# Kernel optimization log

Hardware: AMD Instinct MI355X
Metric: run time of the kernel (lower is better)

Reference implementation:

```python
import jax, jax.numpy as jnp
import numpy as np

N = 50000
DIN, DH, DOUT = 128, 128, 64
DEPTH = 3
TEMP = 1.0
WEIGHT = 0.5
LN_EPS = 1e-5
E_RAND = 1_600_000


def setup_inputs() -> dict:
    key = jax.random.key(0)
    ks = jax.random.split(key, 16)
    x = jax.random.normal(ks[0], (N, DIN), jnp.float32)
    # random edges + ring (guarantees degree >= 2 after symmetrization)
    src = jax.random.randint(ks[1], (E_RAND,), 0, N)
    dst = jax.random.randint(ks[2], (E_RAND,), 0, N)
    ring = jnp.arange(N)
    s = jnp.concatenate([src, ring])
    d = jnp.concatenate([dst, (ring + 1) % N])
    edge_index = jnp.stack([jnp.concatenate([s, d]), jnp.concatenate([d, s])]).astype(jnp.int64)  # [2, 3.3M], symmetric

    def glorot(k, i, o):
        return jax.random.normal(k, (i, o), jnp.float32) * jnp.sqrt(2.0 / (i + o)).astype(jnp.float32)

    return {
        "x": x, "edge_index": edge_index,
        "W0": glorot(ks[3], DIN, DH), "b0": jnp.zeros((DH,), jnp.float32),
        "W1": glorot(ks[4], DH, DH),  "b1": jnp.zeros((DH,), jnp.float32),
        "W2": glorot(ks[5], DH, DH),  "b2": jnp.zeros((DH,), jnp.float32),
        "W_out": glorot(ks[6], DH, DOUT), "b_out": jnp.zeros((DOUT,), jnp.float32),
        "gamma": jnp.ones((DH,), jnp.float32), "beta": jnp.zeros((DH,), jnp.float32),
    }


def _seg(vals, idx):
    return jax.ops.segment_sum(vals, idx, num_segments=N)


def _gcn_conv(h_in, W, b, src, dst):
    # PyG GCNConv: self-loops, sym norm D^-1/2 (A+I) D^-1/2
    h = h_in @ W
    ones = jnp.ones(src.shape, jnp.float32)
    deg = _seg(ones, dst) + 1.0  # degree incl. self-loop
    dinv = jax.lax.rsqrt(deg)
    msg = h[src] * (dinv[src] * dinv[dst])[:, None]
    return _seg(msg, dst) + h * (1.0 / deg)[:, None] + b


def _layernorm(x, g, b):
    m = jnp.mean(x, axis=-1, keepdims=True)
    v = jnp.mean((x - m) ** 2, axis=-1, keepdims=True)
    return (x - m) * jax.lax.rsqrt(v + LN_EPS) * g + b


def reference(x, edge_index, W0, b0, W1, b1, W2, b2, W_out, b_out, gamma, beta):
    src, dst = edge_index[0], edge_index[1]
    h = x
    for W, b in ((W0, b0), (W1, b1), (W2, b2)):
        h = _layernorm(jax.nn.relu(_gcn_conv(h, W, b, src, dst)), gamma, beta)
    emb = _gcn_conv(h, W_out, b_out, src, dst)  # [N, DOUT]

    # --- entropy gradient (edge-list form of the dense-A einsums) ---
    ones = jnp.ones(src.shape, jnp.float32)
    deg_adj = _seg(ones, src)                     # row sums of A (no self-loops)
    en_norm = 1.0 / jnp.sqrt(deg_adj * DH)        # uses hidden_dim, as in the original

    rn2 = jnp.sum(emb * emb, axis=1)              # ||X_i||^2
    dot = jnp.sum(emb[src] * emb[dst], axis=1)    # <X_i, X_j> per edge
    res1 = deg_adj * rn2
    res2 = _seg(dot, src)
    res3 = _seg(rn2[dst], src)
    energies = 0.5 * (res1 - 2.0 * res2 + res3) * en_norm  # normalize_energies=True

    logits = -energies / TEMP
    P = jax.nn.softmax(logits, axis=0) + 1e-10
    logP = jnp.log(P)
    S = -jnp.sum(P * logP)
    Pbar = P * (S + logP)                         # [N]

    nsumX = _seg(emb[dst], src)                   # sum_j A_ij X_j
    nsumP = _seg(Pbar[dst], src)                  # sum_j A_ij Pbar_j
    XP = emb * Pbar[:, None]
    g1 = deg_adj[:, None] * XP
    g2 = emb * nsumP[:, None]
    g3 = Pbar[:, None] * nsumX
    g4 = _seg(XP[dst], src)
    grad_S = (g1 + g2 - g3 - g4) / TEMP * en_norm[:, None]

    return emb + WEIGHT * grad_S
```

## Files before the change

### kernel.cpp

```cpp
#include <hip/hip_runtime.h>

#define DIN 128
#define DH  128
#define DFO 64
#define LN_EPS 1e-5f
#define WEIGHT 0.5f

#define MAXB  104
#define CAPB  64
#define FLUSH 32
#define SENT  0xFFFFFFFFu

typedef unsigned int uint32;

__device__ __forceinline__ float bf_lo(uint32 u) { return __uint_as_float(u << 16); }
__device__ __forceinline__ float bf_hi(uint32 u) { return __uint_as_float(u & 0xFFFF0000u); }
__device__ __forceinline__ uint32 pack_bf16(float a, float b) {
  uint32 ua = __float_as_uint(a), ub = __float_as_uint(b);
  ua += 0x7FFFu + ((ua >> 16) & 1u);
  ub += 0x7FFFu + ((ub >> 16) & 1u);
  return (ua >> 16) | (ub & 0xFFFF0000u);
}

__device__ __forceinline__ float wave_sum(float v) {
  #pragma unroll
  for (int off = 32; off > 0; off >>= 1) v += __shfl_xor(v, off);
  return v;
}
__device__ __forceinline__ float wave_max(float v) {
  #pragma unroll
  for (int off = 32; off > 0; off >>= 1) v = fmaxf(v, __shfl_xor(v, off));
  return v;
}

__device__ __forceinline__ void acc8(float* a, uint4 u) {
  a[0] += bf_lo(u.x); a[1] += bf_hi(u.x);
  a[2] += bf_lo(u.y); a[3] += bf_hi(u.y);
  a[4] += bf_lo(u.z); a[5] += bf_hi(u.z);
  a[6] += bf_lo(u.w); a[7] += bf_hi(u.w);
}
__device__ __forceinline__ void fma8(float* a, uint4 u, float p) {
  a[0] = fmaf(bf_lo(u.x), p, a[0]); a[1] = fmaf(bf_hi(u.x), p, a[1]);
  a[2] = fmaf(bf_lo(u.y), p, a[2]); a[3] = fmaf(bf_hi(u.y), p, a[3]);
  a[4] = fmaf(bf_lo(u.z), p, a[4]); a[5] = fmaf(bf_hi(u.z), p, a[5]);
  a[6] = fmaf(bf_lo(u.w), p, a[6]); a[7] = fmaf(bf_hi(u.w), p, a[7]);
}

__global__ __launch_bounds__(256) void k_bin3(const int* __restrict__ src, const int* __restrict__ dst,
                       int E2, int nbc, int GCAP, int* __restrict__ gbcnt,
                       uint32* __restrict__ gpairs) {
  __shared__ uint32 lbuf[MAXB][CAPB];
  __shared__ int lcnt[MAXB];
  __shared__ int fbase[MAXB];
  __shared__ int fm[MAXB];
  __shared__ short flist[MAXB];
  __shared__ int fn;
  int wv = threadIdx.x >> 6, ln = threadIdx.x & 63;
  for (int b = threadIdx.x; b < nbc; b += 256) lcnt[b] = 0;
  __syncthreads();

  for (int base = blockIdx.x * 256; base < E2; base += gridDim.x * 256) {
    int i = base + threadIdx.x;
    if (i < E2) {
      int s = src[i], d = dst[i];
      int b0 = s >> 9;
      uint32 v0 = ((uint32)(s & 511) << 16) | (uint32)d;
      int sl = atomicAdd(&lcnt[b0], 1);
      if (sl < CAPB) lbuf[b0][sl] = v0;
      else { int g = atomicAdd(&gbcnt[b0 * 16], 1); gpairs[(size_t)b0 * GCAP + g] = v0; }
      int b1 = d >> 9;
      uint32 v1 = ((uint32)(d & 511) << 16) | (uint32)s;
      sl = atomicAdd(&lcnt[b1], 1);
      if (sl < CAPB) lbuf[b1][sl] = v1;
      else { int g = atomicAdd(&gbcnt[b1 * 16], 1); gpairs[(size_t)b1 * GCAP + g] = v1; }
    }
    if (threadIdx.x == 0) fn = 0;
    __syncthreads();
    if (threadIdx.x < nbc) {
      int m = lcnt[threadIdx.x];
      if (m >= FLUSH) {
        if (m > CAPB) m = CAPB;
        int r = (m + 15) & ~15;
        fbase[threadIdx.x] = atomicAdd(&gbcnt[threadIdx.x * 16], r);
        fm[threadIdx.x] = m;
        int fi = atomicAdd(&fn, 1);
        flist[fi] = (short)threadIdx.x;
      }
    }
    __syncthreads();
    int nf = fn;
    for (int fi = wv; fi < nf; fi += 4) {
      int b = flist[fi];
      int m = fm[b], r = (m + 15) & ~15, g = fbase[b];
      if (ln < r)
        gpairs[(size_t)b * GCAP + g + ln] = (ln < m) ? lbuf[b][ln] : SENT;
    }
    __syncthreads();
    if (threadIdx.x < nbc && lcnt[threadIdx.x] >= FLUSH) lcnt[threadIdx.x] = 0;
    __syncthreads();
  }
  if (threadIdx.x < nbc) {
    int m = lcnt[threadIdx.x]; if (m > CAPB) m = CAPB;
    fm[threadIdx.x] = m;
    if (m > 0) {
      int r = (m + 15) & ~15;
      fbase[threadIdx.x] = atomicAdd(&gbcnt[threadIdx.x * 16], r);
    }
  }
  __syncthreads();
  for (int b = wv; b < nbc; b += 4) {
    int m = fm[b];
    if (m > 0) {
      int r = (m + 15) & ~15, g = fbase[b];
      if (ln < r)
        gpairs[(size_t)b * GCAP + g + ln] = (ln < m) ? lbuf[b][ln] : SENT;
    }
  }
}

__global__ __launch_bounds__(1024) void k_csr(const uint32* __restrict__ gpairs, const int* __restrict__ gbcnt,
                      int GCAP, int GCAPC, int N, int* __restrict__ rowbeg, int* __restrict__ rowcnt,
                      float* __restrict__ dinv, float* __restrict__ cntf, int* __restrict__ col) {
  __shared__ int hist[512];
  __shared__ int pos[512];
  int b = blockIdx.x, tid = threadIdx.x;
  if (tid < 512) hist[tid] = 0;
  __syncthreads();
  int m = gbcnt[b * 16];
  const uint32* pp = gpairs + (size_t)b * GCAP;
  for (int t = tid; t < m; t += 1024) {
    uint32 v = pp[t];
    if (v != SENT) atomicAdd(&hist[v >> 16], 1);
  }
  __syncthreads();
  int cnt = (tid < 512) ? hist[tid] : 0;
  for (int off = 1; off < 512; off <<= 1) {
    int u = (tid >= off && tid < 512) ? hist[tid - off] : 0;
    __syncthreads();
    if (tid < 512) hist[tid] += u;
    __syncthreads();
  }
  int cbase = b * GCAPC;
  if (tid < 512) {
    int excl = hist[tid] - cnt;
    pos[tid] = excl;
    int node = (b << 9) + tid;
    if (node < N) {
      rowbeg[node] = cbase + excl;
      rowcnt[node] = cnt;
      cntf[node] = (float)cnt;
      dinv[node] = rsqrtf((float)cnt + 1.0f);
    }
  }
  __syncthreads();
  for (int t = tid; t < m; t += 1024) {
    uint32 v = pp[t];
    if (v != SENT) {
      int sl = atomicAdd(&pos[v >> 16], 1);
      col[cbase + sl] = (int)(v & 0xFFFFu);
    }
  }
}

template <int COLS, bool BF16A>
__global__ __launch_bounds__(256) void k_gemm_tile(const void* __restrict__ Ap, const float* __restrict__ W,
                            const float* __restrict__ dinv, uint32* __restrict__ outb, int N) {
  const int CG  = COLS / 4;
  const int RG  = 256 / CG;
  const int RPT = 64 / RG;
  __shared__ float4 At4[64 * 32];
  int t = threadIdx.x;
  int rbase = blockIdx.x * 64;
  #pragma unroll
  for (int i2 = 0; i2 < 8; ++i2) {
    int idx = t + 256 * i2;
    int row = idx >> 5, c4i = idx & 31;
    int gr = rbase + row;
    float4 v = make_float4(0.f, 0.f, 0.f, 0.f);
    if (gr < N) {
      if (BF16A) {
        uint2 p = ((const uint2*)Ap)[(size_t)gr * 32 + c4i];
        v = make_float4(bf_lo(p.x), bf_hi(p.x), bf_lo(p.y), bf_hi(p.y));
      } else {
        v = ((const float4*)Ap)[(size_t)gr * 32 + c4i];
      }
    }
    At4[idx] = v;
  }
  __syncthreads();
  int c4 = t % CG, rg = t / CG;
  float acc[RPT][4];
  #pragma unroll
  for (int r = 0; r < RPT; ++r) { acc[r][0] = acc[r][1] = acc[r][2] = acc[r][3] = 0.f; }
  const float4* W4 = (const float4*)W;
  #pragma unroll 2
  for (int k4 = 0; k4 < 32; ++k4) {
    float4 w0 = W4[(k4 * 4 + 0) * CG + c4];
    float4 w1 = W4[(k4 * 4 + 1) * CG + c4];
    float4 w2 = W4[(k4 * 4 + 2) * CG + c4];
    float4 w3 = W4[(k4 * 4 + 3) * CG + c4];
    #pragma unroll
    for (int r = 0; r < RPT; ++r) {
      float4 av = At4[(rg * RPT + r) * 32 + k4];
      acc[r][0] = fmaf(av.x, w0.x, acc[r][0]); acc[r][0] = fmaf(av.y, w1.x, acc[r][0]);
      acc[r][0] = fmaf(av.z, w2.x, acc[r][0]); acc[r][0] = fmaf(av.w, w3.x, acc[r][0]);
      acc[r][1] = fmaf(av.x, w0.y, acc[r][1]); acc[r][1] = fmaf(av.y, w1.y, acc[r][1]);
      acc[r][1] = fmaf(av.z, w2.y, acc[r][1]); acc[r][1] = fmaf(av.w, w3.y, acc[r][1]);
      acc[r][2] = fmaf(av.x, w0.z, acc[r][2]); acc[r][2] = fmaf(av.y, w1.z, acc[r][2]);
      acc[r][2] = fmaf(av.z, w2.z, acc[r][2]); acc[r][2] = fmaf(av.w, w3.z, acc[r][2]);
      acc[r][3] = fmaf(av.x, w0.w, acc[r][3]); acc[r][3] = fmaf(av.y, w1.w, acc[r][3]);
      acc[r][3] = fmaf(av.z, w2.w, acc[r][3]); acc[r][3] = fmaf(av.w, w3.w, acc[r][3]);
    }
  }
  #pragma unroll
  for (int r = 0; r < RPT; ++r) {
    int gr = rbase + rg * RPT + r;
    if (gr < N) {
      float s = dinv[gr];
      uint2 o;
      o.x = pack_bf16(acc[r][0] * s, acc[r][1] * s);
      o.y = pack_bf16(acc[r][2] * s, acc[r][3] * s);
      ((uint2*)outb)[(size_t)gr * CG + c4] = o;
    }
  }
}

__global__ __launch_bounds__(128) void k_agg_ln(const uint4* __restrict__ hsb4, const int* __restrict__ rowbeg,
                         const int* __restrict__ rowcnt, const int* __restrict__ col,
                         const float* __restrict__ dinv, const float* __restrict__ bias,
                         const float* __restrict__ gamma, const float* __restrict__ beta,
                         uint4* __restrict__ hout, int N) {
  int i = blockIdx.x;
  int tid = threadIdx.x;
  int lane = tid & 63;
  int f4 = lane & 15;
  int sl = ((tid >> 6) << 2) | (lane >> 4);
  int beg = rowbeg[i], end = beg + rowcnt[i];
  float a[8] = {0,0,0,0,0,0,0,0}, b[8] = {0,0,0,0,0,0,0,0};
  if (tid < 16) { uint4 u = hsb4[(size_t)i * 16 + f4]; acc8(a, u); }
  int t = beg + sl;
  for (; t + 8 < end; t += 16) {
    int j0 = col[t], j1 = col[t + 8];
    uint4 u0 = hsb4[(size_t)j0 * 16 + f4];
    uint4 u1 = hsb4[(size_t)j1 * 16 + f4];
    acc8(a, u0); acc8(b, u1);
  }
  for (; t < end; t += 8) {
    int j = col[t];
    uint4 u = hsb4[(size_t)j * 16 + f4];
    acc8(a, u);
  }
  #pragma unroll
  for (int k = 0; k < 8; ++k) {
    a[k] += b[k];
    a[k] += __shfl_xor(a[k], 16);
    a[k] += __shfl_xor(a[k], 32);
  }
  __shared__ float4 part[16][2];
  if (tid >= 64 && tid < 80) {
    part[f4][0] = make_float4(a[0], a[1], a[2], a[3]);
    part[f4][1] = make_float4(a[4], a[5], a[6], a[7]);
  }
  __syncthreads();
  if (tid < 16) {
    float4 p0 = part[f4][0], p1 = part[f4][1];
    a[0] += p0.x; a[1] += p0.y; a[2] += p0.z; a[3] += p0.w;
    a[4] += p1.x; a[5] += p1.y; a[6] += p1.z; a[7] += p1.w;
    float di = dinv[i];
    float4 bb0 = ((const float4*)bias)[f4 * 2], bb1 = ((const float4*)bias)[f4 * 2 + 1];
    float v[8];
    v[0] = fmaxf(fmaf(a[0], di, bb0.x), 0.f);
    v[1] = fmaxf(fmaf(a[1], di, bb0.y), 0.f);
    v[2] = fmaxf(fmaf(a[2], di, bb0.z), 0.f);
    v[3] = fmaxf(fmaf(a[3], di, bb0.w), 0.f);
    v[4] = fmaxf(fmaf(a[4], di, bb1.x), 0.f);
    v[5] = fmaxf(fmaf(a[5], di, bb1.y), 0.f);
    v[6] = fmaxf(fmaf(a[6], di, bb1.z), 0.f);
    v[7] = fmaxf(fmaf(a[7], di, bb1.w), 0.f);
    float s = 0.f, s2 = 0.f;
    #pragma unroll
    for (int k = 0; k < 8; ++k) { s += v[k]; s2 += v[k] * v[k]; }
    #pragma unroll
    for (int off = 8; off > 0; off >>= 1) { s += __shfl_xor(s, off); s2 += __shfl_xor(s2, off); }
    float mean = s * (1.f / 128.f);
    float var  = s2 * (1.f / 128.f) - mean * mean;
    float rstd = rsqrtf(var + LN_EPS);
    float4 gg0 = ((const float4*)gamma)[f4 * 2], gg1 = ((const float4*)gamma)[f4 * 2 + 1];
    float4 be0 = ((const float4*)beta)[f4 * 2],  be1 = ((const float4*)beta)[f4 * 2 + 1];
    float g0 = (v[0] - mean) * rstd * gg0.x + be0.x;
    float g1 = (v[1] - mean) * rstd * gg0.y + be0.y;
    float g2 = (v[2] - mean) * rstd * gg0.z + be0.z;
    float g3 = (v[3] - mean) * rstd * gg0.w + be0.w;
    float g4 = (v[4] - mean) * rstd * gg1.x + be1.x;
    float g5 = (v[5] - mean) * rstd * gg1.y + be1.y;
    float g6 = (v[6] - mean) * rstd * gg1.z + be1.z;
    float g7 = (v[7] - mean) * rstd * gg1.w + be1.w;
    uint4 o;
    o.x = pack_bf16(g0, g1); o.y = pack_bf16(g2, g3);
    o.z = pack_bf16(g4, g5); o.w = pack_bf16(g6, g7);
    hout[(size_t)i * 16 + f4] = o;
  }
}

__global__ __launch_bounds__(64) void k_agg_out(const uint4* __restrict__ hso4, const int* __restrict__ rowbeg,
                          const int* __restrict__ rowcnt, const int* __restrict__ col,
                          const float* __restrict__ dinv, const float* __restrict__ bias,
                          float* __restrict__ embf, uint4* __restrict__ embb4,
                          float* __restrict__ rn2, int N) {
  int i = blockIdx.x, lane = threadIdx.x;
  int f4 = lane & 7, sl = lane >> 3;
  int beg = rowbeg[i], end = beg + rowcnt[i];
  float a[8] = {0,0,0,0,0,0,0,0}, b[8] = {0,0,0,0,0,0,0,0};
  if (lane < 8) { uint4 u = hso4[(size_t)i * 8 + f4]; acc8(a, u); }
  int t = beg + sl;
  for (; t + 8 < end; t += 16) {
    int j0 = col[t], j1 = col[t + 8];
    uint4 u0 = hso4[(size_t)j0 * 8 + f4];
    uint4 u1 = hso4[(size_t)j1 * 8 + f4];
    acc8(a, u0); acc8(b, u1);
  }
  for (; t < end; t += 8) {
    uint4 u = hso4[(size_t)col[t] * 8 + f4];
    acc8(a, u);
  }
  #pragma unroll
  for (int k = 0; k < 8; ++k) {
    a[k] += b[k];
    a[k] += __shfl_xor(a[k], 8);
    a[k] += __shfl_xor(a[k], 16);
    a[k] += __shfl_xor(a[k], 32);
  }
  float di = dinv[i];
  float4 bb0 = ((const float4*)bias)[f4 * 2], bb1 = ((const float4*)bias)[f4 * 2 + 1];
  float e[8];
  e[0] = fmaf(a[0], di, bb0.x); e[1] = fmaf(a[1], di, bb0.y);
  e[2] = fmaf(a[2], di, bb0.z); e[3] = fmaf(a[3], di, bb0.w);
  e[4] = fmaf(a[4], di, bb1.x); e[5] = fmaf(a[5], di, bb1.y);
  e[6] = fmaf(a[6], di, bb1.z); e[7] = fmaf(a[7], di, bb1.w);
  float ss = 0.f;
  #pragma unroll
  for (int k = 0; k < 8; ++k) ss += e[k] * e[k];
  ss += __shfl_xor(ss, 1); ss += __shfl_xor(ss, 2); ss += __shfl_xor(ss, 4);
  if (lane == 0) rn2[i] = ss;
  if (lane < 8) {
    ((float4*)embf)[(size_t)i * 16 + f4 * 2]     = make_float4(e[0], e[1], e[2], e[3]);
    ((float4*)embf)[(size_t)i * 16 + f4 * 2 + 1] = make_float4(e[4], e[5], e[6], e[7]);
    uint4 o;
    o.x = pack_bf16(e[0], e[1]); o.y = pack_bf16(e[2], e[3]);
    o.z = pack_bf16(e[4], e[5]); o.w = pack_bf16(e[6], e[7]);
    embb4[(size_t)i * 8 + f4] = o;
  }
}

__global__ __launch_bounds__(64) void k_passA(const float* __restrict__ embf, const uint4* __restrict__ embb4,
                        const int* __restrict__ rowbeg, const int* __restrict__ rowcnt,
                        const int* __restrict__ col, const float* __restrict__ rn2,
                        const float* __restrict__ cntf, float* __restrict__ nsumX,
                        float* __restrict__ logits, int N) {
  int i = blockIdx.x, lane = threadIdx.x;
  int f4 = lane & 7, sl = lane >> 3;
  int beg = rowbeg[i], end = beg + rowcnt[i];
  float a[8] = {0,0,0,0,0,0,0,0}, b[8] = {0,0,0,0,0,0,0,0};
  float r3 = 0.f;
  int t = beg + sl;
  for (; t + 8 < end; t += 16) {
    int j0 = col[t], j1 = col[t + 8];
    uint4 u0 = embb4[(size_t)j0 * 8 + f4];
    uint4 u1 = embb4[(size_t)j1 * 8 + f4];
    acc8(a, u0); acc8(b, u1);
    if (f4 == 0) r3 += rn2[j0] + rn2[j1];
  }
  for (; t < end; t += 8) {
    int j = col[t];
    uint4 u = embb4[(size_t)j * 8 + f4];
    acc8(a, u);
    if (f4 == 0) r3 += rn2[j];
  }
  #pragma unroll
  for (int k = 0; k < 8; ++k) {
    a[k] += b[k];
    a[k] += __shfl_xor(a[k], 8);
    a[k] += __shfl_xor(a[k], 16);
    a[k] += __shfl_xor(a[k], 32);
  }
  r3 += __shfl_xor(r3, 8); r3 += __shfl_xor(r3, 16); r3 += __shfl_xor(r3, 32);
  float4 e0 = ((const float4*)embf)[(size_t)i * 16 + f4 * 2];
  float4 e1 = ((const float4*)embf)[(size_t)i * 16 + f4 * 2 + 1];
  float dd = e0.x * a[0] + e0.y * a[1] + e0.z * a[2] + e0.w * a[3]
           + e1.x * a[4] + e1.y * a[5] + e1.z * a[6] + e1.w * a[7];
  dd += __shfl_xor(dd, 1); dd += __shfl_xor(dd, 2); dd += __shfl_xor(dd, 4);
  r3 += __shfl_xor(r3, 1); r3 += __shfl_xor(r3, 2); r3 += __shfl_xor(r3, 4);
  if (lane < 8) {
    ((float4*)nsumX)[(size_t)i * 16 + f4 * 2]     = make_float4(a[0], a[1], a[2], a[3]);
    ((float4*)nsumX)[(size_t)i * 16 + f4 * 2 + 1] = make_float4(a[4], a[5], a[6], a[7]);
  }
  if (lane == 0) {
    float c = cntf[i];
    float en = rsqrtf(c * 128.0f);
    logits[i] = -0.5f * (c * rn2[i] - 2.f * dd + r3) * en;
  }
}

__global__ __launch_bounds__(256) void k_sm1(const float* __restrict__ logits, int N,
                                             float4* __restrict__ partials) {
  int idx = blockIdx.x * 256 + threadIdx.x;
  int w = threadIdx.x >> 6, ln = threadIdx.x & 63;
  float x = (idx < N) ? logits[idx] : -3.4e38f;
  float m = wave_max(x);
  __shared__ float red[3][4];
  if (ln == 0) red[0][w] = m;
  __syncthreads();
  float M = fmaxf(fmaxf(red[0][0], red[0][1]), fmaxf(red[0][2], red[0][3]));
  float ev = (idx < N) ? expf(x - M) : 0.f;
  float tv = (idx < N) ? (x - M) * ev : 0.f;
  float se = wave_sum(ev), st = wave_sum(tv);
  if (ln == 0) { red[1][w] = se; red[2][w] = st; }
  __syncthreads();
  if (threadIdx.x == 0)
    partials[blockIdx.x] = make_float4(M, red[1][0] + red[1][1] + red[1][2] + red[1][3],
                                          red[2][0] + red[2][1] + red[2][2] + red[2][3], 0.f);
}

__global__ __launch_bounds__(256) void k_sm2(const float4* __restrict__ partials, int nb,
                                             float* __restrict__ scal) {
  int tid = threadIdx.x;
  int w = tid >> 6, ln = tid & 63;
  float4 p = (tid < nb) ? partials[tid] : make_float4(-3.4e38f, 0.f, 0.f, 0.f);
  float m = wave_max(p.x);
  __shared__ float red[3][4];
  if (ln == 0) red[0][w] = m;
  __syncthreads();
  float M = fmaxf(fmaxf(red[0][0], red[0][1]), fmaxf(red[0][2], red[0][3]));
  float sc = (tid < nb) ? expf(p.x - M) : 0.f;
  float se = p.y * sc;
  float tt = (p.z + (p.x - M) * p.y) * sc;
  se = wave_sum(se); tt = wave_sum(tt);
  if (ln == 0) { red[1][w] = se; red[2][w] = tt; }
  __syncthreads();
  if (tid == 0) {
    float SE = red[1][0] + red[1][1] + red[1][2] + red[1][3];
    float TT = red[2][0] + red[2][1] + red[2][2] + red[2][3];
    scal[0] = M;
    scal[1] = SE;
    scal[2] = logf(SE) - TT / SE;
  }
}

__global__ __launch_bounds__(256) void k_pbar(const float* __restrict__ logits, int N,
                     const float* __restrict__ scal, float* __restrict__ Pb) {
  float M = scal[0], SE = scal[1], S = scal[2];
  int i = blockIdx.x * blockDim.x + threadIdx.x;
  int stride = gridDim.x * blockDim.x;
  for (; i < N; i += stride) {
    float p = expf(logits[i] - M) / SE + 1e-10f;
    Pb[i] = p * (S + logf(p));
  }
}

__global__ __launch_bounds__(64) void k_passB(const float* __restrict__ embf, const uint4* __restrict__ embb4,
                        const int* __restrict__ rowbeg, const int* __restrict__ rowcnt,
                        const int* __restrict__ col, const float* __restrict__ Pb,
                        const float* __restrict__ cntf, float* __restrict__ outp, int N) {
  int i = blockIdx.x, lane = threadIdx.x;
  int f4 = lane & 7, sl = lane >> 3;
  int beg = rowbeg[i], end = beg + rowcnt[i];
  float a[8] = {0,0,0,0,0,0,0,0}, b[8] = {0,0,0,0,0,0,0,0};
  float sp = 0.f;
  int t = beg + sl;
  for (; t + 8 < end; t += 16) {
    int j0 = col[t], j1 = col[t + 8];
    float p0 = Pb[j0], p1 = Pb[j1];
    uint4 u0 = embb4[(size_t)j0 * 8 + f4];
    uint4 u1 = embb4[(size_t)j1 * 8 + f4];
    fma8(a, u0, p0); fma8(b, u1, p1);
    if (f4 == 0) sp += p0 + p1;
  }
  for (; t < end; t += 8) {
    int j = col[t];
    float p = Pb[j];
    uint4 u = embb4[(size_t)j * 8 + f4];
    fma8(a, u, p);
    if (f4 == 0) sp += p;
  }
  #pragma unroll
  for (int k = 0; k < 8; ++k) {
    a[k] += b[k];
    a[k] += __shfl_xor(a[k], 8);
    a[k] += __shfl_xor(a[k], 16);
    a[k] += __shfl_xor(a[k], 32);
  }
  sp += __shfl_xor(sp, 8); sp += __shfl_xor(sp, 16); sp += __shfl_xor(sp, 32);
  sp += __shfl_xor(sp, 1); sp += __shfl_xor(sp, 2); sp += __shfl_xor(sp, 4);
  if (lane < 8) {
    float4 e0 = ((const float4*)embf)[(size_t)i * 16 + f4 * 2];
    float4 e1 = ((const float4*)embf)[(size_t)i * 16 + f4 * 2 + 1];
    float4 n0 = ((const float4*)outp)[(size_t)i * 16 + f4 * 2];
    float4 n1 = ((const float4*)outp)[(size_t)i * 16 + f4 * 2 + 1];
    float Pi = Pb[i];
    float c = cntf[i];
    float wgt = WEIGHT * rsqrtf(c * 128.0f);
    float g0 = c * e0.x * Pi + e0.x * sp - Pi * n0.x - a[0];
    float g1 = c * e0.y * Pi + e0.y * sp - Pi * n0.y - a[1];
    float g2 = c * e0.z * Pi + e0.z * sp - Pi * n0.z - a[2];
    float g3 = c * e0.w * Pi + e0.w * sp - Pi * n0.w - a[3];
    float g4 = c * e1.x * Pi + e1.x * sp - Pi * n1.x - a[4];
    float g5 = c * e1.y * Pi + e1.y * sp - Pi * n1.y - a[5];
    float g6 = c * e1.z * Pi + e1.z * sp - Pi * n1.z - a[6];
    float g7 = c * e1.w * Pi + e1.w * sp - Pi * n1.w - a[7];
    ((float4*)outp)[(size_t)i * 16 + f4 * 2] =
        make_float4(fmaf(wgt, g0, e0.x), fmaf(wgt, g1, e0.y), fmaf(wgt, g2, e0.z), fmaf(wgt, g3, e0.w));
    ((float4*)outp)[(size_t)i * 16 + f4 * 2 + 1] =
        make_float4(fmaf(wgt, g4, e1.x), fmaf(wgt, g5, e1.y), fmaf(wgt, g6, e1.z), fmaf(wgt, g7, e1.w));
  }
}

extern "C" void kernel_launch(void* const* d_in, const int* in_sizes, int n_in,
                              void* d_out, int out_size, void* d_ws, size_t ws_size,
                              hipStream_t stream) {
  const float* x     = (const float*)d_in[0];
  const int*   ei    = (const int*)d_in[1];
  const float* W0    = (const float*)d_in[2];
  const float* b0    = (const float*)d_in[3];
  const float* W1    = (const float*)d_in[4];
  const float* b1    = (const float*)d_in[5];
  const float* W2    = (const float*)d_in[6];
  const float* b2    = (const float*)d_in[7];
  const float* Wo    = (const float*)d_in[8];
  const float* bo    = (const float*)d_in[9];
  const float* gamma = (const float*)d_in[10];
  const float* beta  = (const float*)d_in[11];

  int N = in_sizes[0] / DIN;
  int E = in_sizes[1] / 2;
  int E2 = E / 2;
  const int* src = ei;
  const int* dst = ei + E;
  int nbc = (N + 511) >> 9;
  int perb = E / nbc;
  int GCAP  = ((perb + perb / 3 + 8192) + 15) & ~15;
  int GCAPC = perb + 4096;

  char* w = (char*)d_ws;
  auto alloc = [&](size_t bytes) { void* p = w; w += (bytes + 255) & ~(size_t)255; return p; };
  char*   hreg = (char*)alloc((size_t)N * DH * 4);
  uint32* hsb  = (uint32*)alloc((size_t)N * DH * 2);
  uint32* embb = (uint32*)alloc((size_t)N * DFO * 2);
  int*    colx = (int*)alloc((size_t)nbc * GCAPC * 4);
  int*    rowbeg = (int*)alloc((size_t)N * 4);
  int*    rowcnt = (int*)alloc((size_t)N * 4);
  float*  dinv   = (float*)alloc((size_t)N * 4);
  float*  cntf   = (float*)alloc((size_t)N * 4);
  float*  rn2    = (float*)alloc((size_t)N * 4);
  float*  logits = (float*)alloc((size_t)N * 4);
  float*  Pb     = (float*)alloc((size_t)N * 4);
  int*    gbcnt  = (int*)alloc((size_t)MAXB * 16 * 4);
  float4* partials = (float4*)alloc(4096);
  float*  scal   = (float*)alloc(256);

  uint32* gpairs = (uint32*)hreg;
  uint32* h      = (uint32*)hreg;
  float*  embf   = (float*)hreg;

  hipMemsetAsync(gbcnt, 0, (size_t)MAXB * 64, stream);
  k_bin3<<<1024, 256, 0, stream>>>(src, dst, E2, nbc, GCAP, gbcnt, gpairs);
  k_csr<<<nbc, 1024, 0, stream>>>(gpairs, gbcnt, GCAP, GCAPC, N, rowbeg, rowcnt, dinv, cntf, colx);

  int gblk = (N + 63) / 64;

  k_gemm_tile<DH, false><<<gblk, 256, 0, stream>>>(x, W0, dinv, hsb, N);
  k_agg_ln<<<N, 128, 0, stream>>>((const uint4*)hsb, rowbeg, rowcnt, colx, dinv, b0, gamma, beta, (uint4*)h, N);
  k_gemm_tile<DH, true><<<gblk, 256, 0, stream>>>(h, W1, dinv, hsb, N);
  k_agg_ln<<<N, 128, 0, stream>>>((const uint4*)hsb, rowbeg, rowcnt, colx, dinv, b1, gamma, beta, (uint4*)h, N);
  k_gemm_tile<DH, true><<<gblk, 256, 0, stream>>>(h, W2, dinv, hsb, N);
  k_agg_ln<<<N, 128, 0, stream>>>((const uint4*)hsb, rowbeg, rowcnt, colx, dinv, b2, gamma, beta, (uint4*)h, N);

  k_gemm_tile<DFO, true><<<gblk, 256, 0, stream>>>(h, Wo, dinv, hsb, N);
  k_agg_out<<<N, 64, 0, stream>>>((const uint4*)hsb, rowbeg, rowcnt, colx, dinv, bo, embf, (uint4*)embb, rn2, N);

  k_passA<<<N, 64, 0, stream>>>(embf, (const uint4*)embb, rowbeg, rowcnt, colx, rn2, cntf, (float*)d_out, logits, N);
  int nb = (N + 255) / 256;
  k_sm1<<<nb, 256, 0, stream>>>(logits, N, partials);
  k_sm2<<<1, 256, 0, stream>>>(partials, nb, scal);
  k_pbar<<<256, 256, 0, stream>>>(logits, N, scal, Pb);
  k_passB<<<N, 64, 0, stream>>>(embf, (const uint4*)embb, rowbeg, rowcnt, colx, Pb, cntf, (float*)d_out, N);
}
```

Before: 669.8 us.

## Split feature gathers into column planes and fold LayerNorm into next GEMM

Feature rows are stored as two 64-column bf16 planes, and each aggregation runs as two passes, one per plane. The idea is that each gather pass touches a smaller working set that fits better in cache. LayerNorm is no longer applied in the aggregation kernel; it stores the pre-norm ReLU output plus per-row sum statistics. The following GEMM then applies mean/rstd algebraically, using gamma-scaled weights and gamma/beta column sums precomputed by a new prep kernel. This doubles the number of aggregation launches and re-reads the col indices for each plane, and normalizing after the GEMM slightly changes the rounding.

```diff
diff --git a/kernel.cpp b/kernel.cpp
--- a/kernel.cpp
+++ b/kernel.cpp
@@ -44,6 +44,27 @@
   a[2] = fmaf(bf_lo(u.y), p, a[2]); a[3] = fmaf(bf_hi(u.y), p, a[3]);
   a[4] = fmaf(bf_lo(u.z), p, a[4]); a[5] = fmaf(bf_hi(u.z), p, a[5]);
   a[6] = fmaf(bf_lo(u.w), p, a[6]); a[7] = fmaf(bf_hi(u.w), p, a[7]);
+}
+
+__global__ __launch_bounds__(64) void k_prep(const float* __restrict__ g, const float* __restrict__ b,
+                      const float* __restrict__ W1, const float* __restrict__ W2,
+                      const float* __restrict__ Wo, float* __restrict__ Wg1,
+                      float* __restrict__ Wg2, float* __restrict__ Wgo,
+                      float* __restrict__ vecs) {
+  int c = blockIdx.x * 64 + threadIdx.x;
+  const float* W; float* Wg; float* gv; float* bv; int ld; int col;
+  if (c < 128)      { W = W1; Wg = Wg1; gv = vecs;       bv = vecs + 128; ld = 128; col = c; }
+  else if (c < 256) { W = W2; Wg = Wg2; gv = vecs + 256; bv = vecs + 384; ld = 128; col = c - 128; }
+  else              { W = Wo; Wg = Wgo; gv = vecs + 512; bv = vecs + 576; ld = 64;  col = c - 256; }
+  float gs = 0.f, bs = 0.f;
+  for (int k = 0; k < 128; ++k) {
+    float w = W[k * ld + col];
+    float gk = g[k];
+    Wg[k * ld + col] = gk * w;
+    gs += gk * w;
+    bs += b[k] * w;
+  }
+  gv[col] = gs; bv[col] = bs;
 }
 
 __global__ __launch_bounds__(256) void k_bin3(const int* __restrict__ src, const int* __restrict__ dst,
@@ -162,12 +183,15 @@
   }
 }
 
-template <int COLS, bool BF16A>
-__global__ __launch_bounds__(256) void k_gemm_tile(const void* __restrict__ Ap, const float* __restrict__ W,
-                            const float* __restrict__ dinv, uint32* __restrict__ outb, int N) {
+template <int COLS, int MODE>
+__global__ __launch_bounds__(256) void k_gemm(const void* __restrict__ Ap, const float* __restrict__ W,
+                            const float* __restrict__ dinv, const float2* __restrict__ stats,
+                            const float* __restrict__ gW, const float* __restrict__ bW,
+                            uint32* __restrict__ outb, int N) {
   const int CG  = COLS / 4;
   const int RG  = 256 / CG;
   const int RPT = 64 / RG;
+  const int OPL = CG / 2;
   __shared__ float4 At4[64 * 32];
   int t = threadIdx.x;
   int rbase = blockIdx.x * 64;
@@ -178,8 +202,9 @@
     int gr = rbase + row;
     float4 v = make_float4(0.f, 0.f, 0.f, 0.f);
     if (gr < N) {
-      if (BF16A) {
-        uint2 p = ((const uint2*)Ap)[(size_t)gr * 32 + c4i];
+      if (MODE == 1) {
+        const uint2* A2 = (const uint2*)Ap;
+        uint2 p = A2[(size_t)(c4i >> 4) * N * 16 + (size_t)gr * 16 + (c4i & 15)];
         v = make_float4(bf_lo(p.x), bf_hi(p.x), bf_lo(p.y), bf_hi(p.y));
       } else {
         v = ((const float4*)Ap)[(size_t)gr * 32 + c4i];
@@ -212,93 +237,93 @@
       acc[r][3] = fmaf(av.z, w2.w, acc[r][3]); acc[r][3] = fmaf(av.w, w3.w, acc[r][3]);
     }
   }
+  float4 g4 = make_float4(0.f, 0.f, 0.f, 0.f), b4 = make_float4(0.f, 0.f, 0.f, 0.f);
+  if (MODE == 1) { g4 = ((const float4*)gW)[c4]; b4 = ((const float4*)bW)[c4]; }
   #pragma unroll
   for (int r = 0; r < RPT; ++r) {
     int gr = rbase + rg * RPT + r;
     if (gr < N) {
       float s = dinv[gr];
+      float o0, o1, o2, o3;
+      if (MODE == 1) {
+        float2 st = stats[gr];
+        o0 = s * (st.y * (acc[r][0] - st.x * g4.x) + b4.x);
+        o1 = s * (st.y * (acc[r][1] - st.x * g4.y) + b4.y);
+        o2 = s * (st.y * (acc[r][2] - st.x * g4.z) + b4.z);
+        o3 = s * (st.y * (acc[r][3] - st.x * g4.w) + b4.w);
+      } else {
+        o0 = acc[r][0] * s; o1 = acc[r][1] * s; o2 = acc[r][2] * s; o3 = acc[r][3] * s;
+      }
       uint2 o;
-      o.x = pack_bf16(acc[r][0] * s, acc[r][1] * s);
-      o.y = pack_bf16(acc[r][2] * s, acc[r][3] * s);
-      ((uint2*)outb)[(size_t)gr * CG + c4] = o;
-    }
-  }
-}
-
-__global__ __launch_bounds__(128) void k_agg_ln(const uint4* __restrict__ hsb4, const int* __restrict__ rowbeg,
-                         const int* __restrict__ rowcnt, const int* __restrict__ col,
-                         const float* __restrict__ dinv, const float* __restrict__ bias,
-                         const float* __restrict__ gamma, const float* __restrict__ beta,
-                         uint4* __restrict__ hout, int N) {
-  int i = blockIdx.x;
-  int tid = threadIdx.x;
-  int lane = tid & 63;
-  int f4 = lane & 15;
-  int sl = ((tid >> 6) << 2) | (lane >> 4);
+      o.x = pack_bf16(o0, o1);
+      o.y = pack_bf16(o2, o3);
+      int pl = c4 / OPL, slot = c4 % OPL;
+      ((uint2*)outb)[(size_t)pl * N * OPL + (size_t)gr * OPL + slot] = o;
+    }
+  }
+}
+
+template <int PLANE>
+__global__ __launch_bounds__(64) void k_aggh(const uint4* __restrict__ hsb4, const int* __restrict__ rowbeg,
+                      const int* __restrict__ rowcnt, const int* __restrict__ col,
+                      const float* __restrict__ dinv, const float* __restrict__ bias,
+                      uint4* __restrict__ vb4, float2* __restrict__ ss,
+                      float2* __restrict__ stats, int N) {
+  int i = blockIdx.x, lane = threadIdx.x;
+  int f = lane & 7, sl = lane >> 3;
+  const uint4* hp = hsb4 + (size_t)PLANE * N * 8;
   int beg = rowbeg[i], end = beg + rowcnt[i];
   float a[8] = {0,0,0,0,0,0,0,0}, b[8] = {0,0,0,0,0,0,0,0};
-  if (tid < 16) { uint4 u = hsb4[(size_t)i * 16 + f4]; acc8(a, u); }
+  if (lane < 8) acc8(a, hp[(size_t)i * 8 + f]);
   int t = beg + sl;
   for (; t + 8 < end; t += 16) {
     int j0 = col[t], j1 = col[t + 8];
-    uint4 u0 = hsb4[(size_t)j0 * 16 + f4];
-    uint4 u1 = hsb4[(size_t)j1 * 16 + f4];
+    uint4 u0 = hp[(size_t)j0 * 8 + f];
+    uint4 u1 = hp[(size_t)j1 * 8 + f];
     acc8(a, u0); acc8(b, u1);
   }
-  for (; t < end; t += 8) {
-    int j = col[t];
-    uint4 u = hsb4[(size_t)j * 16 + f4];
-    acc8(a, u);
-  }
+  for (; t < end; t += 8) acc8(a, hp[(size_t)col[t] * 8 + f]);
   #pragma unroll
   for (int k = 0; k < 8; ++k) {
     a[k] += b[k];
+    a[k] += __shfl_xor(a[k], 8);
     a[k] += __shfl_xor(a[k], 16);
     a[k] += __shfl_xor(a[k], 32);
   }
-  __shared__ float4 part[16][2];
-  if (tid >= 64 && tid < 80) {
-    part[f4][0] = make_float4(a[0], a[1], a[2], a[3]);
-    part[f4][1] = make_float4(a[4], a[5], a[6], a[7]);
-  }
-  __syncthreads();
-  if (tid < 16) {
-    float4 p0 = part[f4][0], p1 = part[f4][1];
-    a[0] += p0.x; a[1] += p0.y; a[2] += p0.z; a[3] += p0.w;
-    a[4] += p1.x; a[5] += p1.y; a[6] += p1.z; a[7] += p1.w;
-    float di = dinv[i];
-    float4 bb0 = ((const float4*)bias)[f4 * 2], bb1 = ((const float4*)bias)[f4 * 2 + 1];
-    float v[8];
-    v[0] = fmaxf(fmaf(a[0], di, bb0.x), 0.f);
-    v[1] = fmaxf(fmaf(a[1], di, bb0.y), 0.f);
-    v[2] = fmaxf(fmaf(a[2], di, bb0.z), 0.f);
-    v[3] = fmaxf(fmaf(a[3], di, bb0.w), 0.f);
-    v[4] = fmaxf(fmaf(a[4], di, bb1.x), 0.f);
-    v[5] = fmaxf(fmaf(a[5], di, bb1.y), 0.f);
-    v[6] = fmaxf(fmaf(a[6], di, bb1.z), 0.f);
-    v[7] = fmaxf(fmaf(a[7], di, bb1.w), 0.f);
-    float s = 0.f, s2 = 0.f;
-    #pragma unroll
-    for (int k = 0; k < 8; ++k) { s += v[k]; s2 += v[k] * v[k]; }
-    #pragma unroll
-    for (int off = 8; off > 0; off >>= 1) { s += __shfl_xor(s, off); s2 += __shfl_xor(s2, off); }
-    float mean = s * (1.f / 128.f);
-    float var  = s2 * (1.f / 128.f) - mean * mean;
-    float rstd = rsqrtf(var + LN_EPS);
-    float4 gg0 = ((const float4*)gamma)[f4 * 2], gg1 = ((const float4*)gamma)[f4 * 2 + 1];
-    float4 be0 = ((const float4*)beta)[f4 * 2],  be1 = ((const float4*)beta)[f4 * 2 + 1];
-    float g0 = (v[0] - mean) * rstd * gg0.x + be0.x;
-    float g1 = (v[1] - mean) * rstd * gg0.y + be0.y;
-    float g2 = (v[2] - mean) * rstd * gg0.z + be0.z;
-    float g3 = (v[3] - mean) * rstd * gg0.w + be0.w;
-    float g4 = (v[4] - mean) * rstd * gg1.x + be1.x;
-    float g5 = (v[5] - mean) * rstd * gg1.y + be1.y;
-    float g6 = (v[6] - mean) * rstd * gg1.z + be1.z;
-    float g7 = (v[7] - mean) * rstd * gg1.w + be1.w;
+  float di = dinv[i];
+  const float4* bb = (const float4*)(bias + PLANE * 64);
+  float4 bb0 = bb[f * 2], bb1 = bb[f * 2 + 1];
+  float v[8];
+  v[0] = fmaxf(fmaf(a[0], di, bb0.x), 0.f);
+  v[1] = fmaxf(fmaf(a[1], di, bb0.y), 0.f);
+  v[2] = fmaxf(fmaf(a[2], di, bb0.z), 0.f);
+  v[3] = fmaxf(fmaf(a[3], di, bb0.w), 0.f);
+  v[4] = fmaxf(fmaf(a[4], di, bb1.x), 0.f);
+  v[5] = fmaxf(fmaf(a[5], di, bb1.y), 0.f);
+  v[6] = fmaxf(fmaf(a[6], di, bb1.z), 0.f);
+  v[7] = fmaxf(fmaf(a[7], di, bb1.w), 0.f);
+  float s = 0.f, s2 = 0.f;
+  #pragma unroll
+  for (int k = 0; k < 8; ++k) { s += v[k]; s2 += v[k] * v[k]; }
+  s += __shfl_xor(s, 1); s2 += __shfl_xor(s2, 1);
+  s += __shfl_xor(s, 2); s2 += __shfl_xor(s2, 2);
+  s += __shfl_xor(s, 4); s2 += __shfl_xor(s2, 4);
+  if (lane < 8) {
     uint4 o;
-    o.x = pack_bf16(g0, g1); o.y = pack_bf16(g2, g3);
-    o.z = pack_bf16(g4, g5); o.w = pack_bf16(g6, g7);
-    hout[(size_t)i * 16 + f4] = o;
+    o.x = pack_bf16(v[0], v[1]); o.y = pack_bf16(v[2], v[3]);
+    o.z = pack_bf16(v[4], v[5]); o.w = pack_bf16(v[6], v[7]);
+    vb4[(size_t)PLANE * N * 8 + (size_t)i * 8 + f] = o;
+  }
+  if (lane == 0) {
+    if (PLANE == 0) {
+      ss[i] = make_float2(s, s2);
+    } else {
+      float2 q = ss[i];
+      float S = s + q.x, S2 = s2 + q.y;
+      float mean = S * (1.f / 128.f);
+      float var = S2 * (1.f / 128.f) - mean * mean;
+      stats[i] = make_float2(mean, rsqrtf(var + LN_EPS));
+    }
   }
 }
 
@@ -309,20 +334,19 @@
                           float* __restrict__ rn2, int N) {
   int i = blockIdx.x, lane = threadIdx.x;
   int f4 = lane & 7, sl = lane >> 3;
+  const uint4* hp = hso4 + (size_t)(f4 >> 2) * N * 4;
+  int fs = f4 & 3;
   int beg = rowbeg[i], end = beg + rowcnt[i];
   float a[8] = {0,0,0,0,0,0,0,0}, b[8] = {0,0,0,0,0,0,0,0};
-  if (lane < 8) { uint4 u = hso4[(size_t)i * 8 + f4]; acc8(a, u); }
+  if (lane < 8) acc8(a, hp[(size_t)i * 4 + fs]);
   int t = beg + sl;
   for (; t + 8 < end; t += 16) {
     int j0 = col[t], j1 = col[t + 8];
-    uint4 u0 = hso4[(size_t)j0 * 8 + f4];
-    uint4 u1 = hso4[(size_t)j1 * 8 + f4];
+    uint4 u0 = hp[(size_t)j0 * 4 + fs];
+    uint4 u1 = hp[(size_t)j1 * 4 + fs];
     acc8(a, u0); acc8(b, u1);
   }
-  for (; t < end; t += 8) {
-    uint4 u = hso4[(size_t)col[t] * 8 + f4];
-    acc8(a, u);
-  }
+  for (; t < end; t += 8) acc8(a, hp[(size_t)col[t] * 4 + fs]);
   #pragma unroll
   for (int k = 0; k < 8; ++k) {
     a[k] += b[k];
@@ -542,9 +566,8 @@
 
   char* w = (char*)d_ws;
   auto alloc = [&](size_t bytes) { void* p = w; w += (bytes + 255) & ~(size_t)255; return p; };
-  char*   hreg = (char*)alloc((size_t)N * DH * 4);
-  uint32* hsb  = (uint32*)alloc((size_t)N * DH * 2);
-  uint32* embb = (uint32*)alloc((size_t)N * DFO * 2);
+  char*   regA = (char*)alloc((size_t)N * 128 * 2);
+  char*   regB = (char*)alloc((size_t)N * 128 * 2);
   int*    colx = (int*)alloc((size_t)nbc * GCAPC * 4);
   int*    rowbeg = (int*)alloc((size_t)N * 4);
   int*    rowcnt = (int*)alloc((size_t)N * 4);
@@ -553,34 +576,46 @@
   float*  rn2    = (float*)alloc((size_t)N * 4);
   float*  logits = (float*)alloc((size_t)N * 4);
   float*  Pb     = (float*)alloc((size_t)N * 4);
+  float2* ss     = (float2*)alloc((size_t)N * 8);
+  float2* stats  = (float2*)alloc((size_t)N * 8);
+  float*  Wg1    = (float*)alloc(128 * 128 * 4);
+  float*  Wg2    = (float*)alloc(128 * 128 * 4);
+  float*  Wgo    = (float*)alloc(128 * 64 * 4);
+  float*  vecs   = (float*)alloc(640 * 4);
   int*    gbcnt  = (int*)alloc((size_t)MAXB * 16 * 4);
   float4* partials = (float4*)alloc(4096);
   float*  scal   = (float*)alloc(256);
 
-  uint32* gpairs = (uint32*)hreg;
-  uint32* h      = (uint32*)hreg;
-  float*  embf   = (float*)hreg;
+  uint32* gpairs = (uint32*)regA;
+  uint4*  vb4    = (uint4*)regA;
+  float*  embf   = (float*)regA;
+  uint4*  hsb4   = (uint4*)regB;
+  uint32* hso    = (uint32*)regB;
+  uint4*  embb4  = (uint4*)(regB + (size_t)N * 64 * 2);
 
   hipMemsetAsync(gbcnt, 0, (size_t)MAXB * 64, stream);
+  k_prep<<<5, 64, 0, stream>>>(gamma, beta, W1, W2, Wo, Wg1, Wg2, Wgo, vecs);
   k_bin3<<<1024, 256, 0, stream>>>(src, dst, E2, nbc, GCAP, gbcnt, gpairs);
   k_csr<<<nbc, 1024, 0, stream>>>(gpairs, gbcnt, GCAP, GCAPC, N, rowbeg, rowcnt, dinv, cntf, colx);
 
   int gblk = (N + 63) / 64;
 
-  k_gemm_tile<DH, false><<<gblk, 256, 0, stream>>>(x, W0, dinv, hsb, N);
-  k_agg_ln<<<N, 128, 0, stream>>>((const uint4*)hsb, rowbeg, rowcnt, colx, dinv, b0, gamma, beta, (uint4*)h, N);
-  k_gemm_tile<DH, true><<<gblk, 256, 0, stream>>>(h, W1, dinv, hsb, N);
-  k_agg_ln<<<N, 128, 0, stream>>>((const uint4*)hsb, rowbeg, rowcnt, colx, dinv, b1, gamma, beta, (uint4*)h, N);
-  k_gemm_tile<DH, true><<<gblk, 256, 0, stream>>>(h, W2, dinv, hsb, N);
-  k_agg_ln<<<N, 128, 0, stream>>>((const uint4*)hsb, rowbeg, rowcnt, colx, dinv, b2, gamma, beta, (uint4*)h, N);
-
-  k_gemm_tile<DFO, true><<<gblk, 256, 0, stream>>>(h, Wo, dinv, hsb, N);
-  k_agg_out<<<N, 64, 0, stream>>>((const uint4*)hsb, rowbeg, rowcnt, colx, dinv, bo, embf, (uint4*)embb, rn2, N);
-
-  k_passA<<<N, 64, 0, stream>>>(embf, (const uint4*)embb, rowbeg, rowcnt, colx, rn2, cntf, (float*)d_out, logits, N);
+  k_gemm<DH, 0><<<gblk, 256, 0, stream>>>(x, W0, dinv, nullptr, nullptr, nullptr, (uint32*)hsb4, N);
+  k_aggh<0><<<N, 64, 0, stream>>>(hsb4, rowbeg, rowcnt, colx, dinv, b0, vb4, ss, stats, N);
+  k_aggh<1><<<N, 64, 0, stream>>>(hsb4, rowbeg, rowcnt, colx, dinv, b0, vb4, ss, stats, N);
+  k_gemm<DH, 1><<<gblk, 256, 0, stream>>>(vb4, Wg1, dinv, stats, vecs, vecs + 128, (uint32*)hsb4, N);
+  k_aggh<0><<<N, 64, 0, stream>>>(hsb4, rowbeg, rowcnt, colx, dinv, b1, vb4, ss, stats, N);
+  k_aggh<1><<<N, 64, 0, stream>>>(hsb4, rowbeg, rowcnt, colx, dinv, b1, vb4, ss, stats, N);
+  k_gemm<DH, 1><<<gblk, 256, 0, stream>>>(vb4, Wg2, dinv, stats, vecs + 256, vecs + 384, (uint32*)hsb4, N);
+  k_aggh<0><<<N, 64, 0, stream>>>(hsb4, rowbeg, rowcnt, colx, dinv, b2, vb4, ss, stats, N);
+  k_aggh<1><<<N, 64, 0, stream>>>(hsb4, rowbeg, rowcnt, colx, dinv, b2, vb4, ss, stats, N);
+  k_gemm<DFO, 1><<<gblk, 256, 0, stream>>>(vb4, Wgo, dinv, stats, vecs + 512, vecs + 576, hso, N);
+  k_agg_out<<<N, 64, 0, stream>>>((const uint4*)hso, rowbeg, rowcnt, colx, dinv, bo, embf, embb4, rn2, N);
+
+  k_passA<<<N, 64, 0, stream>>>(embf, embb4, rowbeg, rowcnt, colx, rn2, cntf, (float*)d_out, logits, N);
   int nb = (N + 255) / 256;
   k_sm1<<<nb, 256, 0, stream>>>(logits, N, partials);
   k_sm2<<<1, 256, 0, stream>>>(partials, nb, scal);
   k_pbar<<<256, 256, 0, stream>>>(logits, N, scal, Pb);
-  k_passB<<<N, 64, 0, stream>>>(embf, (const uint4*)embb, rowbeg, rowcnt, colx, Pb, cntf, (float*)d_out, N);
-}
+  k_passB<<<N, 64, 0, stream>>>(embf, embb4, rowbeg, rowcnt, colx, Pb, cntf, (float*)d_out, N);
+}
```

New measurement: 665.1 us. No clear change (-0.7%).
